# Optimization experiments

Hardware: AMD Instinct MI355X
Metric: run time of the kernel (lower is better)

Reference implementation:

```python
import jax, jax.numpy as jnp
import numpy as np

N_NODES = 100000
N_EDGES = 1600000
D_IN = 128
D_HID = 128
D_OUT = 128
N_LAYERS = 4


def setup_inputs() -> dict:
    key = jax.random.key(0)
    ks = jax.random.split(key, 8)
    x = jax.random.normal(ks[0], (N_NODES, D_IN), dtype=jnp.float32)
    edge_index = jax.random.randint(ks[1], (2, N_EDGES), 0, N_NODES, dtype=jnp.int64)
    s = 1.0 / np.sqrt(D_IN)
    # All layers are 128->128, so stack weights: [L, in, out]
    W_lin = jax.random.uniform(ks[2], (N_LAYERS, D_IN, D_HID), minval=-s, maxval=s, dtype=jnp.float32)
    W_film = jax.random.uniform(ks[3], (N_LAYERS, D_IN, 2 * D_HID), minval=-s, maxval=s, dtype=jnp.float32)
    b_film = jax.random.uniform(ks[4], (N_LAYERS, 2 * D_HID), minval=-s, maxval=s, dtype=jnp.float32)
    W_skip = jax.random.uniform(ks[5], (N_LAYERS, D_IN, D_HID), minval=-s, maxval=s, dtype=jnp.float32)
    W_fskip = jax.random.uniform(ks[6], (N_LAYERS, D_IN, 2 * D_HID), minval=-s, maxval=s, dtype=jnp.float32)
    return {"x": x, "edge_index": edge_index, "W_lin": W_lin, "W_film": W_film,
            "b_film": b_film, "W_skip": W_skip, "W_fskip": W_fskip}


def _film_conv(x, src, dst, deg_inv, W_l, W_f, b_f, W_s, W_fs, c):
    # skip path: FiLM-modulated self transform
    bg_s = x @ W_fs                       # [N, 2C], no bias
    beta_s, gamma_s = bg_s[:, :c], bg_s[:, c:]
    out = jax.nn.relu(gamma_s * (x @ W_s) + beta_s)
    # message path: FiLM params from target node, features from source node
    bg = x @ W_f + b_f                    # [N, 2C]
    beta, gamma = bg[:, :c], bg[:, c:]
    h = x @ W_l                           # [N, C]
    msg = jax.nn.relu(gamma[dst] * h[src] + beta[dst])  # [E, C]
    agg = jax.ops.segment_sum(msg, dst, num_segments=x.shape[0]) * deg_inv  # mean aggr
    return out + agg


def reference(x, edge_index, W_lin, W_film, b_film, W_skip, W_fskip):
    src, dst = edge_index[0], edge_index[1]
    n = x.shape[0]
    deg = jax.ops.segment_sum(jnp.ones((src.shape[0],), x.dtype), dst, num_segments=n)
    deg_inv = (1.0 / jnp.maximum(deg, 1.0))[:, None]   # clamp(min=1) like PyG mean
    for l in range(N_LAYERS):
        x = _film_conv(x, src, dst, deg_inv, W_lin[l], W_film[l], b_film[l],
                       W_skip[l], W_fskip[l], D_HID)
        if l < N_LAYERS - 1:
            x = jax.nn.relu(x)
    return x
```

## Files before the change

kernel.cpp:

```cpp
#include <hip/hip_runtime.h>
#include <hip/hip_bf16.h>

#define N_NODES 100000
#define N_PAD   100096
#define N_EDGES 1600000
#define NXCD    8
#define NRANGE  ((N_NODES + NXCD - 1) / NXCD)
#define NSLICE  256
#define MTILES  (N_PAD / 128)
#define MTQ     ((MTILES + 7) / 8)
#define GEMM_GRID (8 * 7 * MTQ)

typedef __bf16 bf16x8 __attribute__((ext_vector_type(8)));
typedef float  f32x4  __attribute__((ext_vector_type(4)));

__device__ __forceinline__ void gload16(const void* g, void* s) {
    __builtin_amdgcn_global_load_lds(
        (const __attribute__((address_space(1))) unsigned int*)g,
        (__attribute__((address_space(3))) unsigned int*)s, 16, 0, 0);
}

__device__ __forceinline__ float2 bf2f(unsigned p) {
    float2 r;
    union { unsigned u; float f; } a, b;
    a.u = p << 16;
    b.u = p & 0xffff0000u;
    r.x = a.f; r.y = b.f;
    return r;
}
__device__ __forceinline__ unsigned f2bf2(float x, float y) {
    unsigned lo = (unsigned)__builtin_bit_cast(unsigned short, __float2bfloat16(x));
    unsigned hi = (unsigned)__builtin_bit_cast(unsigned short, __float2bfloat16(y));
    return lo | (hi << 16);
}

__global__ void detect_kernel(const unsigned* __restrict__ e, int* __restrict__ flag) {
    __shared__ int nz;
    if (threadIdx.x == 0) nz = 0;
    __syncthreads();
    int local = 0;
    for (int i = threadIdx.x; i < 1024; i += blockDim.x)
        if (e[2 * i + 1] != 0) local = 1;
    if (local) atomicOr(&nz, 1);
    __syncthreads();
    if (threadIdx.x == 0) *flag = (nz == 0) ? 1 : 0;
}

__device__ __forceinline__ int edge_at(const unsigned* __restrict__ e, long idx, int is64) {
    return (int)(is64 ? e[2 * idx] : e[idx]);
}

__global__ __launch_bounds__(256) void hist2_kernel(
    const unsigned* __restrict__ e, const int* __restrict__ flag,
    int* __restrict__ counts) {
    const int r     = blockIdx.x & (NXCD - 1);
    const int slice = blockIdx.x >> 3;
    const int lo = r * NRANGE;
    const int hi = min(lo + NRANGE, N_NODES);
    const int is64 = *flag;
    const int per = (N_EDGES + NSLICE - 1) / NSLICE;
    const int i0 = slice * per;
    const int i1 = min(i0 + per, N_EDGES);
    for (int i = i0 + (int)threadIdx.x; i < i1; i += 256) {
        int d = edge_at(e, (long)N_EDGES + i, is64);
        if (d >= lo && d < hi) atomicAdd(&counts[d], 1);
    }
}

__global__ void scan1_kernel(const int* __restrict__ counts, int* __restrict__ blockSums) {
    __shared__ int red[256];
    int base = blockIdx.x * 1024;
    int sum = 0;
    for (int i = threadIdx.x; i < 1024; i += 256) {
        int idx = base + i;
        sum += (idx < N_NODES) ? counts[idx] : 0;
    }
    red[threadIdx.x] = sum;
    __syncthreads();
    for (int s = 128; s > 0; s >>= 1) {
        if (threadIdx.x < s) red[threadIdx.x] += red[threadIdx.x + s];
        __syncthreads();
    }
    if (threadIdx.x == 0) blockSums[blockIdx.x] = red[0];
}

__global__ void scan2_kernel(int* __restrict__ blockSums, int nb, int* __restrict__ row_ptr) {
    int run = 0;
    for (int i = 0; i < nb; ++i) { int v = blockSums[i]; blockSums[i] = run; run += v; }
    row_ptr[N_NODES] = run;
}

__global__ void scan3_kernel(const int* __restrict__ counts, const int* __restrict__ blockSums,
                             int* __restrict__ row_ptr, int* __restrict__ cursor,
                             float* __restrict__ deg_inv) {
    __shared__ int lds[256];
    int base = blockIdx.x * 1024;
    int t = threadIdx.x;
    int v[4];
    int s = 0;
    for (int i = 0; i < 4; ++i) {
        int idx = base + t * 4 + i;
        v[i] = (idx < N_NODES) ? counts[idx] : 0;
        s += v[i];
    }
    lds[t] = s;
    __syncthreads();
    for (int off = 1; off < 256; off <<= 1) {
        int add = (t >= off) ? lds[t - off] : 0;
        __syncthreads();
        lds[t] += add;
        __syncthreads();
    }
    int excl = lds[t] - s + blockSums[blockIdx.x];
    for (int i = 0; i < 4; ++i) {
        int idx = base + t * 4 + i;
        if (idx < N_NODES) {
            row_ptr[idx] = excl;
            cursor[idx]  = excl;
            deg_inv[idx] = 1.0f / fmaxf((float)v[i], 1.0f);
            excl += v[i];
        }
    }
}

__global__ __launch_bounds__(256) void fill2_kernel(
    const unsigned* __restrict__ e, const int* __restrict__ flag,
    int* __restrict__ cursor, int* __restrict__ csr_src) {
    const int r     = blockIdx.x & (NXCD - 1);
    const int slice = blockIdx.x >> 3;
    const int lo = r * NRANGE;
    const int hi = min(lo + NRANGE, N_NODES);
    const int is64 = *flag;
    const int per = (N_EDGES + NSLICE - 1) / NSLICE;
    const int i0 = slice * per;
    const int i1 = min(i0 + per, N_EDGES);
    for (int i = i0 + (int)threadIdx.x; i < i1; i += 256) {
        int d = edge_at(e, (long)N_EDGES + i, is64);
        if (d >= lo && d < hi) {
            int s = edge_at(e, (long)i, is64);
            int pos = atomicAdd(&cursor[d], 1);
            csr_src[pos] = s;
        }
    }
}

__global__ void bt_prep_kernel(const float* __restrict__ Wl, const float* __restrict__ Wf,
                               const float* __restrict__ Ws, const float* __restrict__ Wfs,
                               __hip_bfloat16* __restrict__ Bt) {
    int idx = blockIdx.x * 256 + threadIdx.x;
    if (idx >= 4 * 768 * 128) return;
    int k   = idx % 128;
    int row = (idx / 128) % 768;
    int lay = idx / (128 * 768);
    float w;
    if (row < 128) {
        w = Wl[(size_t)lay * 16384 + k * 128 + row];
    } else if (row < 384) {
        w = Wf[(size_t)lay * 32768 + k * 256 + (row - 128)];
    } else {
        int rr = row - 384;
        int g = rr >> 4, within = rr & 15;
        int kind = g % 3;
        int c = (g / 3) * 16 + within;
        if (kind == 0)      w = Ws [(size_t)lay * 16384 + k * 128 + c];
        else if (kind == 1) w = Wfs[(size_t)lay * 32768 + k * 256 + c];
        else                w = Wfs[(size_t)lay * 32768 + k * 256 + 128 + c];
    }
    Bt[idx] = __float2bfloat16(w);
}

__global__ void cast_kernel(const float* __restrict__ x, unsigned* __restrict__ A2) {
    long i = (long)blockIdx.x * 256 + threadIdx.x;
    if (i >= (long)N_NODES * 64) return;
    float2 v = ((const float2*)x)[i];
    A2[i] = f2bf2(v.x, v.y);
}

__global__ __launch_bounds__(256, 2) void fused_gemm_kernel(
    const __hip_bfloat16* __restrict__ A,
    const __hip_bfloat16* __restrict__ Bt,
    const float* __restrict__ bfilm,
    __hip_bfloat16* __restrict__ hbuf,
    __hip_bfloat16* __restrict__ bgbuf,
    __hip_bfloat16* __restrict__ skbh)
{
    __shared__ alignas(16) unsigned char lds_raw[32768];
    unsigned char* ldsA = lds_raw;
    unsigned char* ldsB = lds_raw + 16384;

    const int b   = blockIdx.x;
    const int r8  = b & 7;
    const int q   = b >> 3;
    const int jt  = q % 7;
    const int mt  = (q / 7) * 8 + r8;
    if (mt >= MTILES) return;

    const int t  = threadIdx.x;
    const long node0 = (long)mt * 128;
    const int w  = t >> 6, l = t & 63;
    const int wm = w >> 1, wn = w & 1;
    const int lr = l & 15;
    const int kq16 = (l >> 4) << 4;
    const int sw = (lr & 7) << 4;

    const int sr  = t >> 3;
    const int scb = (t & 7) << 4;
    const int scbs = scb ^ ((sr & 7) << 4);

    const char* Abase = (const char*)A;

    if (jt < 3) {
        const char* Bbase = (const char*)Bt + (size_t)(jt * 128) * 256;
        f32x4 acc[4][4];
        #pragma unroll
        for (int mi = 0; mi < 4; ++mi)
            #pragma unroll
            for (int ni = 0; ni < 4; ++ni)
                #pragma unroll
                for (int j = 0; j < 4; ++j) acc[mi][ni][j] = 0.f;

        #pragma unroll
        for (int ks = 0; ks < 2; ++ks) {
            const int k0 = ks * 64;
            #pragma unroll
            for (int i = 0; i < 4; ++i) {
                const int r = (i << 5) + sr;
                gload16(Abase + (node0 + r) * 256 + (size_t)k0 * 2 + scbs,
                        ldsA + (((i << 8) + t) << 4));
                gload16(Bbase + (size_t)r * 256 + (size_t)k0 * 2 + scbs,
                        ldsB + (((i << 8) + t) << 4));
            }
            __syncthreads();

            #pragma unroll
            for (int kh = 0; kh < 2; ++kh) {
                const int kbs = ((kh << 6) + kq16) ^ sw;
                bf16x8 af[4], bfr[4];
                #pragma unroll
                for (int mi = 0; mi < 4; ++mi)
                    af[mi] = *(const bf16x8*)(ldsA + (wm * 64 + mi * 16 + lr) * 128 + kbs);
                #pragma unroll
                for (int ni = 0; ni < 4; ++ni)
                    bfr[ni] = *(const bf16x8*)(ldsB + (wn * 64 + ni * 16 + lr) * 128 + kbs);
                #pragma unroll
                for (int mi = 0; mi < 4; ++mi)
                    #pragma unroll
                    for (int ni = 0; ni < 4; ++ni)
                        acc[mi][ni] = __builtin_amdgcn_mfma_f32_16x16x32_bf16(
                            af[mi], bfr[ni], acc[mi][ni], 0, 0, 0);
            }
            __syncthreads();
        }

        const int col = lr;
        const int rb  = (l >> 4) << 2;
        if (jt == 0) {
            #pragma unroll
            for (int mi = 0; mi < 4; ++mi)
                #pragma unroll
                for (int ni = 0; ni < 4; ++ni) {
                    const int n = wn * 64 + ni * 16 + col;
                    #pragma unroll
                    for (int j = 0; j < 4; ++j) {
                        long node = node0 + wm * 64 + mi * 16 + rb + j;
                        if (node < N_NODES)
                            hbuf[node * 128 + n] = __float2bfloat16(acc[mi][ni][j]);
                    }
                }
        } else {
            const int c0 = (jt - 1) * 128;
            #pragma unroll
            for (int mi = 0; mi < 4; ++mi)
                #pragma unroll
                for (int ni = 0; ni < 4; ++ni) {
                    const int n = wn * 64 + ni * 16 + col;
                    const float bb = bfilm[c0 + n];
                    #pragma unroll
                    for (int j = 0; j < 4; ++j) {
                        long node = node0 + wm * 64 + mi * 16 + rb + j;
                        if (node < N_NODES)
                            bgbuf[node * 256 + c0 + n] = __float2bfloat16(acc[mi][ni][j] + bb);
                    }
                }
        }
    } else {
        const int jt2 = jt - 3;
        const char* Bbase = (const char*)Bt + (size_t)(384 + jt2 * 96) * 256;
        f32x4 acc[4][3];
        #pragma unroll
        for (int mi = 0; mi < 4; ++mi)
            #pragma unroll
            for (int ni = 0; ni < 3; ++ni)
                #pragma unroll
                for (int j = 0; j < 4; ++j) acc[mi][ni][j] = 0.f;

        #pragma unroll
        for (int ks = 0; ks < 2; ++ks) {
            const int k0 = ks * 64;
            #pragma unroll
            for (int i = 0; i < 4; ++i) {
                const int r = (i << 5) + sr;
                gload16(Abase + (node0 + r) * 256 + (size_t)k0 * 2 + scbs,
                        ldsA + (((i << 8) + t) << 4));
            }
            #pragma unroll
            for (int i = 0; i < 3; ++i) {
                const int r = (i << 5) + sr;
                gload16(Bbase + (size_t)r * 256 + (size_t)k0 * 2 + scbs,
                        ldsB + (((i << 8) + t) << 4));
            }
            __syncthreads();

            #pragma unroll
            for (int kh = 0; kh < 2; ++kh) {
                const int kbs = ((kh << 6) + kq16) ^ sw;
                bf16x8 af[4], bfr[3];
                #pragma unroll
                for (int mi = 0; mi < 4; ++mi)
                    af[mi] = *(const bf16x8*)(ldsA + (wm * 64 + mi * 16 + lr) * 128 + kbs);
                #pragma unroll
                for (int ni = 0; ni < 3; ++ni)
                    bfr[ni] = *(const bf16x8*)(ldsB + (wn * 48 + ni * 16 + lr) * 128 + kbs);
                #pragma unroll
                for (int mi = 0; mi < 4; ++mi)
                    #pragma unroll
                    for (int ni = 0; ni < 3; ++ni)
                        acc[mi][ni] = __builtin_amdgcn_mfma_f32_16x16x32_bf16(
                            af[mi], bfr[ni], acc[mi][ni], 0, 0, 0);
            }
            __syncthreads();
        }

        const int c  = (2 * jt2 + wn) * 16 + lr;
        const int rb = (l >> 4) << 2;
        #pragma unroll
        for (int mi = 0; mi < 4; ++mi)
            #pragma unroll
            for (int j = 0; j < 4; ++j) {
                long node = node0 + wm * 64 + mi * 16 + rb + j;
                if (node < N_NODES) {
                    float o = fmaxf(acc[mi][2][j] * acc[mi][0][j] + acc[mi][1][j], 0.f);
                    skbh[node * 128 + c] = __float2bfloat16(o);
                }
            }
    }
}

__global__ __launch_bounds__(256) void agg_kernel(
    const uint2* __restrict__ h22,
    const uint2* __restrict__ bgu2,
    const int* __restrict__ row_ptr, const int* __restrict__ csr_src,
    const float* __restrict__ deg_inv,
    const uint2* __restrict__ sku2,
    uint2* __restrict__ An2,
    float4* __restrict__ fo4)
{
    const int t = threadIdx.x;
    const int v = blockIdx.x * 4 + (t >> 6);
    const int l = t & 63;
    const int half = l >> 5;
    const unsigned c = l & 31;

    const uint2 bu = bgu2[(size_t)v * 64 + c];
    const uint2 gu = bgu2[(size_t)v * 64 + 32 + c];
    const float2 be01 = bf2f(bu.x), be23 = bf2f(bu.y);
    const float2 ga01 = bf2f(gu.x), ga23 = bf2f(gu.y);
    const float dinv = deg_inv[v];

    const int b = row_ptr[v];
    const int e = row_ptr[v + 1];
    const int ne = e - b;
    const int npair = ne >> 1;

    f32x4 ac0 = {0,0,0,0}, ac1 = {0,0,0,0}, ac2 = {0,0,0,0}, ac3 = {0,0,0,0};

    const int* cp = csr_src + b + half;

#define ACC(A_, P_) do {                                   \
        float2 h01 = bf2f((P_).x), h23 = bf2f((P_).y);     \
        (A_)[0] += fmaxf(ga01.x * h01.x + be01.x, 0.f);    \
        (A_)[1] += fmaxf(ga01.y * h01.y + be01.y, 0.f);    \
        (A_)[2] += fmaxf(ga23.x * h23.x + be23.x, 0.f);    \
        (A_)[3] += fmaxf(ga23.y * h23.y + be23.y, 0.f);    \
    } while (0)

    int pi = 0;
    for (; pi + 8 <= npair; pi += 8) {
        unsigned s[8];
        uint2 p[8];
        #pragma unroll
        for (int u = 0; u < 8; ++u) s[u] = (unsigned)cp[2 * (pi + u)];
        #pragma unroll
        for (int u = 0; u < 8; ++u) p[u] = h22[s[u] * 32u + c];
        ACC(ac0, p[0]); ACC(ac1, p[1]); ACC(ac2, p[2]); ACC(ac3, p[3]);
        ACC(ac0, p[4]); ACC(ac1, p[5]); ACC(ac2, p[6]); ACC(ac3, p[7]);
    }
    for (; pi + 4 <= npair; pi += 4) {
        unsigned s[4];
        uint2 p[4];
        #pragma unroll
        for (int u = 0; u < 4; ++u) s[u] = (unsigned)cp[2 * (pi + u)];
        #pragma unroll
        for (int u = 0; u < 4; ++u) p[u] = h22[s[u] * 32u + c];
        ACC(ac0, p[0]); ACC(ac1, p[1]); ACC(ac2, p[2]); ACC(ac3, p[3]);
    }
    for (; pi < npair; ++pi) {
        const unsigned s0 = (unsigned)cp[2 * pi];
        const uint2 p0 = h22[s0 * 32u + c];
        ACC(ac0, p0);
    }
    if ((ne & 1) && half == 0) {
        const unsigned s0 = (unsigned)csr_src[e - 1];
        const uint2 p0 = h22[s0 * 32u + c];
        ACC(ac1, p0);
    }
#undef ACC

    float r0 = (ac0[0] + ac1[0]) + (ac2[0] + ac3[0]);
    float r1 = (ac0[1] + ac1[1]) + (ac2[1] + ac3[1]);
    float r2 = (ac0[2] + ac1[2]) + (ac2[2] + ac3[2]);
    float r3 = (ac0[3] + ac1[3]) + (ac2[3] + ac3[3]);
    r0 += __shfl_xor(r0, 32);
    r1 += __shfl_xor(r1, 32);
    r2 += __shfl_xor(r2, 32);
    r3 += __shfl_xor(r3, 32);

    const uint2 sk = sku2[(size_t)v * 32 + c];
    const float2 s01 = bf2f(sk.x), s23 = bf2f(sk.y);
    const float o0 = s01.x + r0 * dinv;
    const float o1 = s01.y + r1 * dinv;
    const float o2 = s23.x + r2 * dinv;
    const float o3 = s23.y + r3 * dinv;

    if (half == 0) {
        if (An2) {
            An2[(size_t)v * 32 + c] = make_uint2(f2bf2(o0, o1), f2bf2(o2, o3));
        } else {
            fo4[(size_t)v * 32 + c] = make_float4(o0, o1, o2, o3);
        }
    }
}

extern "C" void kernel_launch(void* const* d_in, const int* in_sizes, int n_in,
                              void* d_out, int out_size, void* d_ws, size_t ws_size,
                              hipStream_t stream) {
    const float*    x_in    = (const float*)d_in[0];
    const unsigned* eidx    = (const unsigned*)d_in[1];
    const float*    W_lin   = (const float*)d_in[2];
    const float*    W_film  = (const float*)d_in[3];
    const float*    b_film  = (const float*)d_in[4];
    const float*    W_skip  = (const float*)d_in[5];
    const float*    W_fskip = (const float*)d_in[6];
    float*          out     = (float*)d_out;

    char* ws = (char*)d_ws;
    size_t off = 0;
    auto alloc = [&](size_t bytes) -> void* {
        void* p = ws + off;
        off = (off + bytes + 255) & ~(size_t)255;
        return p;
    };
    int*   flag      = (int*)alloc(4);
    int*   counts    = (int*)alloc((size_t)N_NODES * 4);
    int*   row_ptr   = (int*)alloc((size_t)(N_NODES + 1) * 4);
    int*   cursor    = (int*)alloc((size_t)N_NODES * 4);
    int*   blockSums = (int*)alloc(128 * 4);
    float* deg_inv   = (float*)alloc((size_t)N_NODES * 4);
    int*   csr_src   = (int*)alloc((size_t)N_EDGES * 4);
    __hip_bfloat16* Abuf  = (__hip_bfloat16*)alloc((size_t)N_PAD * 128 * 2);
    __hip_bfloat16* BtAll = (__hip_bfloat16*)alloc((size_t)4 * 768 * 128 * 2);
    __hip_bfloat16* hbuf  = (__hip_bfloat16*)alloc((size_t)N_NODES * 128 * 2);
    __hip_bfloat16* bgbuf = (__hip_bfloat16*)alloc((size_t)N_NODES * 256 * 2);
    __hip_bfloat16* skbh  = (__hip_bfloat16*)alloc((size_t)N_NODES * 128 * 2);
    (void)ws_size; (void)in_sizes; (void)n_in; (void)out_size;

    const int NB_SCAN = (N_NODES + 1023) / 1024;

    hipMemsetAsync(counts, 0, (size_t)N_NODES * 4, stream);
    detect_kernel<<<1, 256, 0, stream>>>(eidx, flag);
    hist2_kernel<<<NXCD * NSLICE, 256, 0, stream>>>(eidx, flag, counts);
    scan1_kernel<<<NB_SCAN, 256, 0, stream>>>(counts, blockSums);
    scan2_kernel<<<1, 1, 0, stream>>>(blockSums, NB_SCAN, row_ptr);
    scan3_kernel<<<NB_SCAN, 256, 0, stream>>>(counts, blockSums, row_ptr, cursor, deg_inv);
    fill2_kernel<<<NXCD * NSLICE, 256, 0, stream>>>(eidx, flag, cursor, csr_src);

    cast_kernel<<<(N_NODES * 64 + 255) / 256, 256, 0, stream>>>(x_in, (unsigned*)Abuf);
    bt_prep_kernel<<<(4 * 768 * 128 + 255) / 256, 256, 0, stream>>>(
        W_lin, W_film, W_skip, W_fskip, BtAll);

    const int AGG_B = N_NODES / 4;
    for (int l = 0; l < 4; ++l) {
        const __hip_bfloat16* Bt_l = BtAll + (size_t)l * 768 * 128;
        fused_gemm_kernel<<<GEMM_GRID, 256, 0, stream>>>(
            Abuf, Bt_l, b_film + (size_t)l * 256, hbuf, bgbuf, skbh);
        agg_kernel<<<AGG_B, 256, 0, stream>>>(
            (const uint2*)hbuf, (const uint2*)bgbuf,
            row_ptr, csr_src, deg_inv, (const uint2*)skbh,
            (l < 3) ? (uint2*)Abuf : (uint2*)nullptr,
            (l == 3) ? (float4*)out : (float4*)nullptr);
    }
}
```

Before: 619.6 us.

## Bucket CSR edges by source range and aggregate 16 nodes per wave by bucket

Edges are first compacted into 32-bit src/dst arrays. The CSR is then built with 8 source-range buckets per destination node, with per-(node,bucket) counts and row pointers. The aggregation kernel now has each wave handle 16 nodes and walk all of them bucket by bucket, so concurrent gathers hit a narrow source range of h for better L2/MALL locality. In exchange there are more preprocessing kernels and bigger index arrays, less per-node parallelism (one wave serialises 16 nodes), and padded nodes now read uninitialised rows.

New measurement: 2.311 ms. 273% more time.

```diff
diff --git a/kernel.cpp b/kernel.cpp
--- a/kernel.cpp
+++ b/kernel.cpp
@@ -8,8 +8,7 @@
 #define NRANGE  ((N_NODES + NXCD - 1) / NXCD)
 #define NSLICE  256
 #define MTILES  (N_PAD / 128)
-#define MTQ     ((MTILES + 7) / 8)
-#define GEMM_GRID (8 * 7 * MTQ)
+#define GEMM_GRID (8 * 7 * (((MTILES) + 7) / 8))
 
 typedef __bf16 bf16x8 __attribute__((ext_vector_type(8)));
 typedef float  f32x4  __attribute__((ext_vector_type(4)));
@@ -50,21 +49,41 @@
     return (int)(is64 ? e[2 * idx] : e[idx]);
 }
 
-__global__ __launch_bounds__(256) void hist2_kernel(
-    const unsigned* __restrict__ e, const int* __restrict__ flag,
-    int* __restrict__ counts) {
+__global__ void compact_kernel(const unsigned* __restrict__ e, const int* __restrict__ flag,
+                               unsigned* __restrict__ src32, unsigned* __restrict__ dst32) {
+    int i = blockIdx.x * 256 + threadIdx.x;
+    if (i >= N_EDGES) return;
+    int is64 = *flag;
+    src32[i] = (unsigned)edge_at(e, (long)i, is64);
+    dst32[i] = (unsigned)edge_at(e, (long)N_EDGES + i, is64);
+}
+
+__global__ __launch_bounds__(256) void hist8_kernel(
+    const unsigned* __restrict__ src32, const unsigned* __restrict__ dst32,
+    int* __restrict__ counts8) {
     const int r     = blockIdx.x & (NXCD - 1);
     const int slice = blockIdx.x >> 3;
-    const int lo = r * NRANGE;
-    const int hi = min(lo + NRANGE, N_NODES);
-    const int is64 = *flag;
+    const unsigned lo = r * NRANGE;
+    const unsigned hi = min((int)lo + NRANGE, N_NODES);
     const int per = (N_EDGES + NSLICE - 1) / NSLICE;
     const int i0 = slice * per;
     const int i1 = min(i0 + per, N_EDGES);
     for (int i = i0 + (int)threadIdx.x; i < i1; i += 256) {
-        int d = edge_at(e, (long)N_EDGES + i, is64);
-        if (d >= lo && d < hi) atomicAdd(&counts[d], 1);
-    }
+        unsigned d = dst32[i];
+        if (d >= lo && d < hi) {
+            unsigned bsrc = src32[i] / NRANGE;
+            atomicAdd(&counts8[(size_t)d * 8 + bsrc], 1);
+        }
+    }
+}
+
+__global__ void sum8_kernel(const int* __restrict__ counts8, int* __restrict__ counts) {
+    int v = blockIdx.x * 256 + threadIdx.x;
+    if (v >= N_NODES) return;
+    int s = 0;
+    #pragma unroll
+    for (int b = 0; b < 8; ++b) s += counts8[(size_t)v * 8 + b];
+    counts[v] = s;
 }
 
 __global__ void scan1_kernel(const int* __restrict__ counts, int* __restrict__ blockSums) {
@@ -91,8 +110,7 @@
 }
 
 __global__ void scan3_kernel(const int* __restrict__ counts, const int* __restrict__ blockSums,
-                             int* __restrict__ row_ptr, int* __restrict__ cursor,
-                             float* __restrict__ deg_inv) {
+                             int* __restrict__ row_ptr, float* __restrict__ deg_inv) {
     __shared__ int lds[256];
     int base = blockIdx.x * 1024;
     int t = threadIdx.x;
@@ -116,30 +134,45 @@
         int idx = base + t * 4 + i;
         if (idx < N_NODES) {
             row_ptr[idx] = excl;
-            cursor[idx]  = excl;
             deg_inv[idx] = 1.0f / fmaxf((float)v[i], 1.0f);
             excl += v[i];
         }
     }
 }
 
-__global__ __launch_bounds__(256) void fill2_kernel(
-    const unsigned* __restrict__ e, const int* __restrict__ flag,
-    int* __restrict__ cursor, int* __restrict__ csr_src) {
+__global__ void rp8_build_kernel(const int* __restrict__ counts8,
+                                 const int* __restrict__ row_ptr,
+                                 int* __restrict__ rp8, int* __restrict__ cursor8) {
+    int v = blockIdx.x * 256 + threadIdx.x;
+    if (v >= N_PAD) return;
+    const int E = row_ptr[N_NODES];
+    int run = (v < N_NODES) ? row_ptr[v] : E;
+    #pragma unroll
+    for (int b = 0; b < 8; ++b) {
+        rp8[(size_t)v * 8 + b]     = run;
+        cursor8[(size_t)v * 8 + b] = run;
+        if (v < N_NODES) run += counts8[(size_t)v * 8 + b];
+    }
+    if (v == N_PAD - 1) rp8[(size_t)N_PAD * 8] = E;
+}
+
+__global__ __launch_bounds__(256) void fill3_kernel(
+    const unsigned* __restrict__ src32, const unsigned* __restrict__ dst32,
+    int* __restrict__ cursor8, int* __restrict__ csr_src) {
     const int r     = blockIdx.x & (NXCD - 1);
     const int slice = blockIdx.x >> 3;
-    const int lo = r * NRANGE;
-    const int hi = min(lo + NRANGE, N_NODES);
-    const int is64 = *flag;
+    const unsigned lo = r * NRANGE;
+    const unsigned hi = min((int)lo + NRANGE, N_NODES);
     const int per = (N_EDGES + NSLICE - 1) / NSLICE;
     const int i0 = slice * per;
     const int i1 = min(i0 + per, N_EDGES);
     for (int i = i0 + (int)threadIdx.x; i < i1; i += 256) {
-        int d = edge_at(e, (long)N_EDGES + i, is64);
+        unsigned d = dst32[i];
         if (d >= lo && d < hi) {
-            int s = edge_at(e, (long)i, is64);
-            int pos = atomicAdd(&cursor[d], 1);
-            csr_src[pos] = s;
+            unsigned s = src32[i];
+            unsigned bsrc = s / NRANGE;
+            int pos = atomicAdd(&cursor8[(size_t)d * 8 + bsrc], 1);
+            csr_src[pos] = (int)s;
         }
     }
 }
@@ -347,96 +380,73 @@
 }
 
 __global__ __launch_bounds__(256) void agg_kernel(
-    const uint2* __restrict__ h22,
-    const uint2* __restrict__ bgu2,
-    const int* __restrict__ row_ptr, const int* __restrict__ csr_src,
+    const unsigned* __restrict__ h_u,
+    const unsigned* __restrict__ bg_u,
+    const int* __restrict__ rp8,
+    const int* __restrict__ csr,
     const float* __restrict__ deg_inv,
-    const uint2* __restrict__ sku2,
-    uint2* __restrict__ An2,
-    float4* __restrict__ fo4)
+    const unsigned* __restrict__ sk_u,
+    unsigned* __restrict__ An_u,
+    float2* __restrict__ fo2)
 {
-    const int t = threadIdx.x;
-    const int v = blockIdx.x * 4 + (t >> 6);
-    const int l = t & 63;
-    const int half = l >> 5;
-    const unsigned c = l & 31;
-
-    const uint2 bu = bgu2[(size_t)v * 64 + c];
-    const uint2 gu = bgu2[(size_t)v * 64 + 32 + c];
-    const float2 be01 = bf2f(bu.x), be23 = bf2f(bu.y);
-    const float2 ga01 = bf2f(gu.x), ga23 = bf2f(gu.y);
-    const float dinv = deg_inv[v];
-
-    const int b = row_ptr[v];
-    const int e = row_ptr[v + 1];
-    const int ne = e - b;
-    const int npair = ne >> 1;
-
-    f32x4 ac0 = {0,0,0,0}, ac1 = {0,0,0,0}, ac2 = {0,0,0,0}, ac3 = {0,0,0,0};
-
-    const int* cp = csr_src + b + half;
-
-#define ACC(A_, P_) do {                                   \
-        float2 h01 = bf2f((P_).x), h23 = bf2f((P_).y);     \
-        (A_)[0] += fmaxf(ga01.x * h01.x + be01.x, 0.f);    \
-        (A_)[1] += fmaxf(ga01.y * h01.y + be01.y, 0.f);    \
-        (A_)[2] += fmaxf(ga23.x * h23.x + be23.x, 0.f);    \
-        (A_)[3] += fmaxf(ga23.y * h23.y + be23.y, 0.f);    \
-    } while (0)
-
-    int pi = 0;
-    for (; pi + 8 <= npair; pi += 8) {
-        unsigned s[8];
-        uint2 p[8];
+    const int w = threadIdx.x >> 6;
+    const int l = threadIdx.x & 63;
+    const int vbase = blockIdx.x * 64 + w * 16;
+
+    unsigned bb[16], gg[16];
+    #pragma unroll
+    for (int i = 0; i < 16; ++i) {
+        const size_t v = (size_t)(vbase + i);
+        bb[i] = bg_u[v * 128 + l];
+        gg[i] = bg_u[v * 128 + 64 + l];
+    }
+    float2 acc[16];
+    #pragma unroll
+    for (int i = 0; i < 16; ++i) acc[i] = make_float2(0.f, 0.f);
+
+    for (int b = 0; b < 8; ++b) {
         #pragma unroll
-        for (int u = 0; u < 8; ++u) s[u] = (unsigned)cp[2 * (pi + u)];
-        #pragma unroll
-        for (int u = 0; u < 8; ++u) p[u] = h22[s[u] * 32u + c];
-        ACC(ac0, p[0]); ACC(ac1, p[1]); ACC(ac2, p[2]); ACC(ac3, p[3]);
-        ACC(ac0, p[4]); ACC(ac1, p[5]); ACC(ac2, p[6]); ACC(ac3, p[7]);
-    }
-    for (; pi + 4 <= npair; pi += 4) {
-        unsigned s[4];
-        uint2 p[4];
-        #pragma unroll
-        for (int u = 0; u < 4; ++u) s[u] = (unsigned)cp[2 * (pi + u)];
-        #pragma unroll
-        for (int u = 0; u < 4; ++u) p[u] = h22[s[u] * 32u + c];
-        ACC(ac0, p[0]); ACC(ac1, p[1]); ACC(ac2, p[2]); ACC(ac3, p[3]);
-    }
-    for (; pi < npair; ++pi) {
-        const unsigned s0 = (unsigned)cp[2 * pi];
-        const uint2 p0 = h22[s0 * 32u + c];
-        ACC(ac0, p0);
-    }
-    if ((ne & 1) && half == 0) {
-        const unsigned s0 = (unsigned)csr_src[e - 1];
-        const uint2 p0 = h22[s0 * 32u + c];
-        ACC(ac1, p0);
-    }
-#undef ACC
-
-    float r0 = (ac0[0] + ac1[0]) + (ac2[0] + ac3[0]);
-    float r1 = (ac0[1] + ac1[1]) + (ac2[1] + ac3[1]);
-    float r2 = (ac0[2] + ac1[2]) + (ac2[2] + ac3[2]);
-    float r3 = (ac0[3] + ac1[3]) + (ac2[3] + ac3[3]);
-    r0 += __shfl_xor(r0, 32);
-    r1 += __shfl_xor(r1, 32);
-    r2 += __shfl_xor(r2, 32);
-    r3 += __shfl_xor(r3, 32);
-
-    const uint2 sk = sku2[(size_t)v * 32 + c];
-    const float2 s01 = bf2f(sk.x), s23 = bf2f(sk.y);
-    const float o0 = s01.x + r0 * dinv;
-    const float o1 = s01.y + r1 * dinv;
-    const float o2 = s23.x + r2 * dinv;
-    const float o3 = s23.y + r3 * dinv;
-
-    if (half == 0) {
-        if (An2) {
-            An2[(size_t)v * 32 + c] = make_uint2(f2bf2(o0, o1), f2bf2(o2, o3));
-        } else {
-            fo4[(size_t)v * 32 + c] = make_float4(o0, o1, o2, o3);
+        for (int i = 0; i < 16; ++i) {
+            const int v = vbase + i;
+            int j        = rp8[(size_t)v * 8 + b];
+            const int j1 = rp8[(size_t)v * 8 + b + 1];
+            const float2 be = bf2f(bb[i]);
+            const float2 ga = bf2f(gg[i]);
+            float2 a0 = make_float2(0.f, 0.f), a1 = make_float2(0.f, 0.f);
+            for (; j + 2 <= j1; j += 2) {
+                const unsigned s0 = (unsigned)csr[j];
+                const unsigned s1 = (unsigned)csr[j + 1];
+                const unsigned p0 = h_u[(size_t)s0 * 64 + l];
+                const unsigned p1 = h_u[(size_t)s1 * 64 + l];
+                const float2 h0 = bf2f(p0), h1 = bf2f(p1);
+                a0.x += fmaxf(ga.x * h0.x + be.x, 0.f);
+                a0.y += fmaxf(ga.y * h0.y + be.y, 0.f);
+                a1.x += fmaxf(ga.x * h1.x + be.x, 0.f);
+                a1.y += fmaxf(ga.y * h1.y + be.y, 0.f);
+            }
+            if (j < j1) {
+                const unsigned s0 = (unsigned)csr[j];
+                const unsigned p0 = h_u[(size_t)s0 * 64 + l];
+                const float2 h0 = bf2f(p0);
+                a0.x += fmaxf(ga.x * h0.x + be.x, 0.f);
+                a0.y += fmaxf(ga.y * h0.y + be.y, 0.f);
+            }
+            acc[i].x += a0.x + a1.x;
+            acc[i].y += a0.y + a1.y;
+        }
+    }
+
+    #pragma unroll
+    for (int i = 0; i < 16; ++i) {
+        const int v = vbase + i;
+        const float dinv = deg_inv[v];
+        const float2 sk = bf2f(sk_u[(size_t)v * 64 + l]);
+        const float o0 = sk.x + acc[i].x * dinv;
+        const float o1 = sk.y + acc[i].y * dinv;
+        if (An_u) {
+            An_u[(size_t)v * 64 + l] = f2bf2(o0, o1);
+        } else if (v < N_NODES) {
+            fo2[(size_t)v * 64 + l] = make_float2(o0, o1);
         }
     }
 }
@@ -462,41 +472,49 @@
     };
     int*   flag      = (int*)alloc(4);
     int*   counts    = (int*)alloc((size_t)N_NODES * 4);
+    int*   counts8   = (int*)alloc((size_t)N_NODES * 8 * 4);
     int*   row_ptr   = (int*)alloc((size_t)(N_NODES + 1) * 4);
-    int*   cursor    = (int*)alloc((size_t)N_NODES * 4);
+    int*   rp8       = (int*)alloc(((size_t)N_PAD * 8 + 1) * 4);
+    int*   cursor8   = (int*)alloc((size_t)N_PAD * 8 * 4);
     int*   blockSums = (int*)alloc(128 * 4);
-    float* deg_inv   = (float*)alloc((size_t)N_NODES * 4);
+    float* deg_inv   = (float*)alloc((size_t)N_PAD * 4);
     int*   csr_src   = (int*)alloc((size_t)N_EDGES * 4);
+    unsigned* src32  = (unsigned*)alloc((size_t)N_EDGES * 4);
+    unsigned* dst32  = (unsigned*)alloc((size_t)N_EDGES * 4);
     __hip_bfloat16* Abuf  = (__hip_bfloat16*)alloc((size_t)N_PAD * 128 * 2);
     __hip_bfloat16* BtAll = (__hip_bfloat16*)alloc((size_t)4 * 768 * 128 * 2);
-    __hip_bfloat16* hbuf  = (__hip_bfloat16*)alloc((size_t)N_NODES * 128 * 2);
-    __hip_bfloat16* bgbuf = (__hip_bfloat16*)alloc((size_t)N_NODES * 256 * 2);
-    __hip_bfloat16* skbh  = (__hip_bfloat16*)alloc((size_t)N_NODES * 128 * 2);
+    __hip_bfloat16* hbuf  = (__hip_bfloat16*)alloc((size_t)N_PAD * 128 * 2);
+    __hip_bfloat16* bgbuf = (__hip_bfloat16*)alloc((size_t)N_PAD * 256 * 2);
+    __hip_bfloat16* skbh  = (__hip_bfloat16*)alloc((size_t)N_PAD * 128 * 2);
     (void)ws_size; (void)in_sizes; (void)n_in; (void)out_size;
 
     const int NB_SCAN = (N_NODES + 1023) / 1024;
-
-    hipMemsetAsync(counts, 0, (size_t)N_NODES * 4, stream);
+    const int EB = (N_EDGES + 255) / 256;
+
+    hipMemsetAsync(counts8, 0, (size_t)N_NODES * 8 * 4, stream);
     detect_kernel<<<1, 256, 0, stream>>>(eidx, flag);
-    hist2_kernel<<<NXCD * NSLICE, 256, 0, stream>>>(eidx, flag, counts);
+    compact_kernel<<<EB, 256, 0, stream>>>(eidx, flag, src32, dst32);
+    hist8_kernel<<<NXCD * NSLICE, 256, 0, stream>>>(src32, dst32, counts8);
+    sum8_kernel<<<(N_NODES + 255) / 256, 256, 0, stream>>>(counts8, counts);
     scan1_kernel<<<NB_SCAN, 256, 0, stream>>>(counts, blockSums);
     scan2_kernel<<<1, 1, 0, stream>>>(blockSums, NB_SCAN, row_ptr);
-    scan3_kernel<<<NB_SCAN, 256, 0, stream>>>(counts, blockSums, row_ptr, cursor, deg_inv);
-    fill2_kernel<<<NXCD * NSLICE, 256, 0, stream>>>(eidx, flag, cursor, csr_src);
+    scan3_kernel<<<NB_SCAN, 256, 0, stream>>>(counts, blockSums, row_ptr, deg_inv);
+    rp8_build_kernel<<<(N_PAD + 255) / 256, 256, 0, stream>>>(counts8, row_ptr, rp8, cursor8);
+    fill3_kernel<<<NXCD * NSLICE, 256, 0, stream>>>(src32, dst32, cursor8, csr_src);
 
     cast_kernel<<<(N_NODES * 64 + 255) / 256, 256, 0, stream>>>(x_in, (unsigned*)Abuf);
     bt_prep_kernel<<<(4 * 768 * 128 + 255) / 256, 256, 0, stream>>>(
         W_lin, W_film, W_skip, W_fskip, BtAll);
 
-    const int AGG_B = N_NODES / 4;
+    const int AGG_B = N_PAD / 64;
     for (int l = 0; l < 4; ++l) {
         const __hip_bfloat16* Bt_l = BtAll + (size_t)l * 768 * 128;
         fused_gemm_kernel<<<GEMM_GRID, 256, 0, stream>>>(
             Abuf, Bt_l, b_film + (size_t)l * 256, hbuf, bgbuf, skbh);
         agg_kernel<<<AGG_B, 256, 0, stream>>>(
-            (const uint2*)hbuf, (const uint2*)bgbuf,
-            row_ptr, csr_src, deg_inv, (const uint2*)skbh,
-            (l < 3) ? (uint2*)Abuf : (uint2*)nullptr,
-            (l == 3) ? (float4*)out : (float4*)nullptr);
-    }
-}
+            (const unsigned*)hbuf, (const unsigned*)bgbuf,
+            rp8, csr_src, deg_inv, (const unsigned*)skbh,
+            (l < 3) ? (unsigned*)Abuf : (unsigned*)nullptr,
+            (l == 3) ? (float2*)out : (float2*)nullptr);
+    }
+}
```
